# Optimization experiments

Hardware: AMD Instinct MI355X
Metric: run time of the kernel (lower is better)

The kernel has to match this reference:

```python
import jax, jax.numpy as jnp
import numpy as np

N_ACC = 100000   # accounts
N_TX = 300000    # transactions
E = 600000       # edges per edge type
H = 256          # hidden_dim
TX_IN = 32
ACC_IN = 16
L = 2            # conv_layers
M = 300000       # edges to classify
BN_EPS = 1e-5


def setup_inputs() -> dict:
    key = jax.random.key(0)
    ks = jax.random.split(key, 24)
    def nrm(k, shape, scale=1.0):
        return jax.random.normal(k, shape, jnp.float32) * scale
    inp = {}
    inp["x_acc"] = nrm(ks[0], (N_ACC, ACC_IN))
    inp["x_tx"] = nrm(ks[1], (N_TX, TX_IN))
    inp["tx_raw"] = nrm(ks[2], (M, TX_IN))
    # edge type account -> transaction (row0: src account, row1: dst transaction)
    inp["ei_sends"] = jnp.stack([jax.random.randint(ks[3], (E,), 0, N_ACC),
                                 jax.random.randint(ks[4], (E,), 0, N_TX)])
    # edge type transaction -> account
    inp["ei_recv"] = jnp.stack([jax.random.randint(ks[5], (E,), 0, N_TX),
                                jax.random.randint(ks[6], (E,), 0, N_ACC)])
    inp["sender_idx"] = jax.random.randint(ks[7], (M,), 0, N_ACC)
    inp["receiver_idx"] = jax.random.randint(ks[8], (M,), 0, N_ACC)
    # input projections (torch Linear: y = x @ W.T + b)
    inp["W_acc"] = nrm(ks[9], (H, ACC_IN), ACC_IN ** -0.5)
    inp["b_acc"] = jnp.zeros((H,), jnp.float32)
    inp["W_tx"] = nrm(ks[10], (H, TX_IN), TX_IN ** -0.5)
    inp["b_tx"] = jnp.zeros((H,), jnp.float32)
    s = H ** -0.5
    # SAGEConv params per layer: _at = acc->tx edge type, _ta = tx->acc edge type
    # Wl: applied to mean-aggregated neighbor messages (has bias), Wr: root/self weight (no bias)
    inp["Wl_at"] = nrm(ks[11], (L, H, H), s); inp["bl_at"] = jnp.zeros((L, H), jnp.float32)
    inp["Wr_at"] = nrm(ks[12], (L, H, H), s)
    inp["Wl_ta"] = nrm(ks[13], (L, H, H), s); inp["bl_ta"] = jnp.zeros((L, H), jnp.float32)
    inp["Wr_ta"] = nrm(ks[14], (L, H, H), s)
    # shared BatchNorm1d per layer (inference mode: running stats)
    inp["bn_gamma"] = jnp.ones((L, H), jnp.float32)
    inp["bn_beta"] = jnp.zeros((L, H), jnp.float32)
    inp["bn_mean"] = nrm(ks[15], (L, H), 0.1)
    inp["bn_var"] = jax.random.uniform(ks[16], (L, H), jnp.float32, 0.5, 1.5)
    # edge MLP: Linear(2H+TX_IN -> H), ReLU, Linear(H -> 1)
    inp["W1"] = nrm(ks[17], (H, 2 * H + TX_IN), (2 * H + TX_IN) ** -0.5)
    inp["b1"] = jnp.zeros((H,), jnp.float32)
    inp["W2"] = nrm(ks[18], (1, H), s)
    inp["b2"] = jnp.zeros((1,), jnp.float32)
    return inp


def _sage(x_src, x_dst, ei, Wl, bl, Wr):
    # PyG SAGEConv: lin_l(mean_{j in N(i)} x_src[j]) + lin_r(x_dst[i])
    src, dst = ei[0], ei[1]
    n_dst = x_dst.shape[0]
    msg = x_src[src]                                                   # [E, H] gather
    agg = jax.ops.segment_sum(msg, dst, num_segments=n_dst)           # [N_dst, H] scatter-add
    cnt = jax.ops.segment_sum(jnp.ones((ei.shape[1],), x_src.dtype), dst, num_segments=n_dst)
    mean = agg / jnp.maximum(cnt, 1.0)[:, None]
    return mean @ Wl.T + bl + x_dst @ Wr.T


def _bn(v, g, b, m, var):
    return (v - m) * (g * jax.lax.rsqrt(var + BN_EPS)) + b


def reference(x_acc, x_tx, tx_raw, ei_sends, ei_recv, sender_idx, receiver_idx,
              W_acc, b_acc, W_tx, b_tx,
              Wl_at, bl_at, Wr_at, Wl_ta, bl_ta, Wr_ta,
              bn_gamma, bn_beta, bn_mean, bn_var,
              W1, b1, W2, b2):
    acc = jax.nn.relu(x_acc @ W_acc.T + b_acc)
    tx = jax.nn.relu(x_tx @ W_tx.T + b_tx)
    for l in range(L):
        # HeteroConv(aggr='sum'): each node type receives from exactly one edge type here
        tx_new = _sage(acc, tx, ei_sends, Wl_at[l], bl_at[l], Wr_at[l])
        acc_new = _sage(tx, acc, ei_recv, Wl_ta[l], bl_ta[l], Wr_ta[l])
        acc = jax.nn.relu(_bn(acc_new, bn_gamma[l], bn_beta[l], bn_mean[l], bn_var[l]))
        tx = jax.nn.relu(_bn(tx_new, bn_gamma[l], bn_beta[l], bn_mean[l], bn_var[l]))
    h_sender = acc[sender_idx]      # [M, H]
    h_receiver = acc[receiver_idx]  # [M, H]
    edge_repr = jnp.concatenate([h_sender, h_receiver, tx_raw], axis=1)  # [M, 2H+TX_IN]
    h = jax.nn.relu(edge_repr @ W1.T + b1)
    return (h @ W2.T + b2)[:, 0]    # [M]
```

## Files before the change

kernel.cpp:

```cpp
#include <hip/hip_runtime.h>
#include <hip/hip_bf16.h>

#define H 256
#define NACC 100000
#define NTX  300000
#define NE   600000
#define NM   300000

typedef unsigned short u16;
typedef unsigned int u32;
typedef __bf16 bf16x8 __attribute__((ext_vector_type(8)));
typedef float f32x4 __attribute__((ext_vector_type(4)));

__device__ __forceinline__ float bf2f(u32 u) {
    union { u32 i; float f; } v; v.i = u << 16; return v.f;
}
__device__ __forceinline__ u16 f2bf(float f) {
    union { float f; u32 i; } v; v.f = f;
    u32 r = v.i + 0x7FFFu + ((v.i >> 16) & 1u);
    return (u16)(r >> 16);
}
__device__ __forceinline__ u32 pk2(float a, float b) {
    return (u32)f2bf(a) | ((u32)f2bf(b) << 16);
}

__global__ void fillz_kernel(u32* __restrict__ p, long long n) {
    long long i = (long long)blockIdx.x * blockDim.x + threadIdx.x;
    long long st = (long long)gridDim.x * blockDim.x;
    for (; i < n; i += st) p[i] = 0u;
}

__global__ void wcat_kernel(const float* __restrict__ Wl, const float* __restrict__ Wr,
                            u16* __restrict__ dst) {
    int c = blockIdx.x, t = threadIdx.x;
    dst[(size_t)c * 512 + t]       = f2bf(Wl[(size_t)c * 256 + t]);
    dst[(size_t)c * 512 + 256 + t] = f2bf(Wr[(size_t)c * 256 + t]);
}
__global__ void w1cvt_kernel(const float* __restrict__ W1, u16* __restrict__ dst) {
    int c = blockIdx.x, t = threadIdx.x;
    for (int k = t; k < 544; k += 256)
        dst[(size_t)c * 544 + k] = f2bf(W1[(size_t)c * 544 + k]);
}
__global__ void wproj_kernel(const float* __restrict__ W, u16* __restrict__ dst, int K) {
    int c = blockIdx.x, t = threadIdx.x;
    dst[(size_t)c * 32 + t] = (t < K) ? f2bf(W[(size_t)c * K + t]) : (u16)0;
}
__global__ void bnprep_kernel(const float* __restrict__ bl, const float* __restrict__ g,
                              const float* __restrict__ be, const float* __restrict__ m,
                              const float* __restrict__ v,
                              float* __restrict__ S, float* __restrict__ B) {
    int c = threadIdx.x;
    float s = g[c] * rsqrtf(v[c] + 1e-5f);
    S[c] = s;
    B[c] = (bl[c] - m[c]) * s + be[c];
}

template <int KK>
__launch_bounds__(256)
__global__ void proj_mfma(const float* __restrict__ x, const u16* __restrict__ Wb,
                          const float* __restrict__ b, u16* __restrict__ out, int N) {
    __shared__ __align__(16) u16 Af[8][64][8];
    __shared__ __align__(16) u16 Bf[16][64][8];
    int tid = threadIdx.x;
    int w = tid >> 6, lane = tid & 63;
    int row0 = blockIdx.x * 128;
    {
        int r = tid >> 1, h = tid & 1;
        int gr = row0 + r;
        int rt = r >> 4, rr = r & 15;
        uint4 p0 = make_uint4(0, 0, 0, 0), p1 = p0;
        if (gr < N && (KK == 32 || h == 0)) {
            const float* xp = x + (size_t)gr * KK + h * 16;
            float4 f0 = *(const float4*)(xp);
            float4 f1 = *(const float4*)(xp + 4);
            float4 f2 = *(const float4*)(xp + 8);
            float4 f3 = *(const float4*)(xp + 12);
            p0 = make_uint4(pk2(f0.x, f0.y), pk2(f0.z, f0.w), pk2(f1.x, f1.y), pk2(f1.z, f1.w));
            p1 = make_uint4(pk2(f2.x, f2.y), pk2(f2.z, f2.w), pk2(f3.x, f3.y), pk2(f3.z, f3.w));
        }
        int kg0 = 2 * h;
        *(uint4*)(&Af[rt][(kg0 * 16 + rr) ^ (kg0 << 2)][0]) = p0;
        *(uint4*)(&Af[rt][((kg0 + 1) * 16 + rr) ^ ((kg0 + 1) << 2)][0]) = p1;
    }
    {
        const u16* wp = Wb + (size_t)tid * 32;
#pragma unroll
        for (int q = 0; q < 4; ++q) {
            uint4 wv = *(const uint4*)(wp + q * 8);
            *(uint4*)(&Bf[tid >> 4][q * 16 + (tid & 15)][0]) = wv;
        }
    }
    __syncthreads();
    int arslot = lane ^ ((lane >> 4) << 2);
    f32x4 acc[8][4];
#pragma unroll
    for (int rt = 0; rt < 8; ++rt) {
        bf16x8 afr = *(const bf16x8*)(&Af[rt][arslot][0]);
#pragma unroll
        for (int ct = 0; ct < 4; ++ct) {
            bf16x8 bfr = *(const bf16x8*)(&Bf[w * 4 + ct][lane][0]);
            acc[rt][ct] = __builtin_amdgcn_mfma_f32_16x16x32_bf16(
                afr, bfr, (f32x4){0.f, 0.f, 0.f, 0.f}, 0, 0, 0);
        }
    }
    int rb = (lane >> 4) * 4, cc = lane & 15;
#pragma unroll
    for (int ct = 0; ct < 4; ++ct) {
        int cg = (w * 4 + ct) * 16 + cc;
        float bv = b[cg];
#pragma unroll
        for (int rt = 0; rt < 8; ++rt)
#pragma unroll
            for (int q = 0; q < 4; ++q) {
                int r = row0 + rt * 16 + rb + q;
                if (r < N)
                    out[(size_t)r * H + cg] = f2bf(fmaxf(acc[rt][ct][q] + bv, 0.0f));
            }
    }
}

__global__ void count_kernel(const int* __restrict__ dst, int E, int* __restrict__ cnt) {
    int e = blockIdx.x * blockDim.x + threadIdx.x;
    if (e < E) atomicAdd(&cnt[dst[e]], 1);
}
__global__ void scan1_kernel(const int* __restrict__ cnt, int N,
                             int* __restrict__ loc, int* __restrict__ bsum) {
    __shared__ int sh[256];
    int b = blockIdx.x, t = threadIdx.x;
    int base = b * 1024 + t * 4;
    int v0 = (base + 0 < N) ? cnt[base + 0] : 0;
    int v1 = (base + 1 < N) ? cnt[base + 1] : 0;
    int v2 = (base + 2 < N) ? cnt[base + 2] : 0;
    int v3 = (base + 3 < N) ? cnt[base + 3] : 0;
    int s = v0 + v1 + v2 + v3;
    sh[t] = s;
    __syncthreads();
    for (int o = 1; o < 256; o <<= 1) {
        int y = (t >= o) ? sh[t - o] : 0;
        __syncthreads();
        sh[t] += y;
        __syncthreads();
    }
    int run = sh[t] - s;
    if (base + 0 < N) loc[base + 0] = run; run += v0;
    if (base + 1 < N) loc[base + 1] = run; run += v1;
    if (base + 2 < N) loc[base + 2] = run; run += v2;
    if (base + 3 < N) loc[base + 3] = run;
    if (t == 0) bsum[b] = sh[255];
}
__global__ void scan2_kernel(int* __restrict__ bsum, int nb) {
    __shared__ int sh[1024];
    int t = threadIdx.x;
    int v = (t < nb) ? bsum[t] : 0;
    sh[t] = v;
    __syncthreads();
    for (int o = 1; o < 1024; o <<= 1) {
        int y = (t >= o) ? sh[t - o] : 0;
        __syncthreads();
        sh[t] += y;
        __syncthreads();
    }
    if (t < nb) bsum[t] = sh[t] - v;
}
__global__ void scan3_kernel(int* __restrict__ ptr, const int* __restrict__ bsum,
                             int N, int total) {
    int i = blockIdx.x * blockDim.x + threadIdx.x;
    if (i < N) ptr[i] += bsum[i >> 10];
    else if (i == N) ptr[N] = total;
}
__global__ void fillcsr_kernel(const int* __restrict__ src, const int* __restrict__ dst, int E,
                               const int* __restrict__ ptr, int* __restrict__ cur,
                               int* __restrict__ perm) {
    int e = blockIdx.x * blockDim.x + threadIdx.x;
    if (e < E) {
        int d = dst[e];
        int pos = ptr[d] + atomicAdd(&cur[d], 1);
        perm[pos] = src[e];
    }
}

template <int WS>
__launch_bounds__(256)
__global__ void gmean_kernel(const u16* __restrict__ feat, int fstride,
                             const int* __restrict__ ptr, const int* __restrict__ perm,
                             u16* __restrict__ out, int ostride, int c0,
                             int rows, int lo) {
    constexpr int LPD = WS / 4;
    constexpr int DPB = 256 / LPD;
    int g = threadIdx.x / LPD;
    int ln = threadIdx.x % LPD;
    int w = blockIdx.x * DPB + g;
    if (w >= rows) return;
    int d = lo + w;
    int e0 = ptr[d], e1 = ptr[d + 1];
    float a0 = 0.f, a1 = 0.f, a2 = 0.f, a3 = 0.f;
    for (int e = e0; e < e1; ++e) {
        int s = perm[e];
        uint2 v = *(const uint2*)(feat + (size_t)s * fstride + (ln << 2));
        a0 += bf2f(v.x & 0xffff); a1 += bf2f(v.x >> 16);
        a2 += bf2f(v.y & 0xffff); a3 += bf2f(v.y >> 16);
    }
    int deg = e1 - e0;
    float sc = (deg > 0) ? (1.0f / (float)deg) : 0.0f;
    uint2 pk;
    pk.x = pk2(a0 * sc, a1 * sc);
    pk.y = pk2(a2 * sc, a3 * sc);
    *(uint2*)(out + (size_t)w * ostride + c0 + (ln << 2)) = pk;
}

template <int K, int NC>
__launch_bounds__(256)
__global__ void proj2_kernel(const float* __restrict__ x, const float* __restrict__ W,
                             const float* __restrict__ b, u16* __restrict__ out,
                             int N, int c0, int ost) {
    __shared__ float xs[128][K + 4];
    constexpr int NG = 512 / NC;
    constexpr int RPT = 128 / NG;
    int tid = threadIdx.x;
    int row0 = blockIdx.x * 128;
    constexpr int NF4 = 128 * K / 4;
    for (int f = tid; f < NF4; f += 256) {
        int r = f / (K / 4), kq = (f % (K / 4)) * 4;
        int gr = row0 + r;
        float4 v = (gr < N) ? *(const float4*)(x + (size_t)gr * K + kq)
                            : make_float4(0.f, 0.f, 0.f, 0.f);
        *(float4*)&xs[r][kq] = v;
    }
    int lt2 = (tid % (NC / 2)) * 2;
    int g = tid / (NC / 2);
    float wa[K], wb[K];
    const float* wpa = W + (size_t)(c0 + lt2) * K;
#pragma unroll
    for (int k = 0; k < K; k += 4) {
        float4 va = *(const float4*)(wpa + k);
        float4 vb = *(const float4*)(wpa + K + k);
        wa[k] = va.x; wa[k + 1] = va.y; wa[k + 2] = va.z; wa[k + 3] = va.w;
        wb[k] = vb.x; wb[k + 1] = vb.y; wb[k + 2] = vb.z; wb[k + 3] = vb.w;
    }
    float b0 = b[c0 + lt2], b1 = b[c0 + lt2 + 1];
    __syncthreads();
#pragma unroll
    for (int rr = 0; rr < RPT; ++rr) {
        int r = g * RPT + rr;
        int gr = row0 + r;
        float a0 = b0, a1 = b1;
#pragma unroll
        for (int k = 0; k < K; k += 4) {
            float4 xv = *(const float4*)&xs[r][k];
            a0 += xv.x * wa[k] + xv.y * wa[k + 1] + xv.z * wa[k + 2] + xv.w * wa[k + 3];
            a1 += xv.x * wb[k] + xv.y * wb[k + 1] + xv.z * wb[k + 2] + xv.w * wb[k + 3];
        }
        if (gr < N) {
            u32 pk = (u32)f2bf(fmaxf(a0, 0.f)) | ((u32)f2bf(fmaxf(a1, 0.f)) << 16);
            *(u32*)(out + (size_t)gr * ost + lt2) = pk;
        }
    }
}

__launch_bounds__(256)
__global__ void combine_gather(const u16* __restrict__ featG, const int* __restrict__ ptr,
                               const int* __restrict__ perm, const u16* __restrict__ xd,
                               const u16* __restrict__ Wcat,
                               const float* __restrict__ bnS, const float* __restrict__ bnB,
                               u16* __restrict__ outF, int rows) {
    __shared__ __align__(16) u16 Am[8][4][64][8];
    __shared__ __align__(16) u16 Af[4][64][8];
    __shared__ __align__(16) u16 Bf[16][64][8];
    int tid = threadIdx.x;
    int w = tid >> 6, lane = tid & 63;
    int row0 = blockIdx.x * 64;

    {
        int r = tid >> 2, g = tid & 3;
        int grow = row0 + r;
        float s[64];
#pragma unroll
        for (int i = 0; i < 64; ++i) s[i] = 0.0f;
        float inv = 0.0f;
        if (grow < rows) {
            int e0 = ptr[grow], e1 = ptr[grow + 1];
            int dg = e1 - e0;
            inv = (dg > 0) ? 1.0f / (float)dg : 0.0f;
            int e = e0;
            for (; e + 1 < e1; e += 2) {
                int n0 = perm[e], n1 = perm[e + 1];
                const u16* p0 = featG + (size_t)n0 * H + g * 64;
                const u16* p1 = featG + (size_t)n1 * H + g * 64;
#pragma unroll
                for (int q = 0; q < 8; ++q) {
                    uint4 v0 = *(const uint4*)(p0 + q * 8);
                    uint4 v1 = *(const uint4*)(p1 + q * 8);
                    s[q * 8 + 0] += bf2f(v0.x & 0xffff) + bf2f(v1.x & 0xffff);
                    s[q * 8 + 1] += bf2f(v0.x >> 16)    + bf2f(v1.x >> 16);
                    s[q * 8 + 2] += bf2f(v0.y & 0xffff) + bf2f(v1.y & 0xffff);
                    s[q * 8 + 3] += bf2f(v0.y >> 16)    + bf2f(v1.y >> 16);
                    s[q * 8 + 4] += bf2f(v0.z & 0xffff) + bf2f(v1.z & 0xffff);
                    s[q * 8 + 5] += bf2f(v0.z >> 16)    + bf2f(v1.z >> 16);
                    s[q * 8 + 6] += bf2f(v0.w & 0xffff) + bf2f(v1.w & 0xffff);
                    s[q * 8 + 7] += bf2f(v0.w >> 16)    + bf2f(v1.w >> 16);
                }
            }
            if (e < e1) {
                int n0 = perm[e];
                const u16* p0 = featG + (size_t)n0 * H + g * 64;
#pragma unroll
                for (int q = 0; q < 8; ++q) {
                    uint4 v0 = *(const uint4*)(p0 + q * 8);
                    s[q * 8 + 0] += bf2f(v0.x & 0xffff);
                    s[q * 8 + 1] += bf2f(v0.x >> 16);
                    s[q * 8 + 2] += bf2f(v0.y & 0xffff);
                    s[q * 8 + 3] += bf2f(v0.y >> 16);
                    s[q * 8 + 4] += bf2f(v0.z & 0xffff);
                    s[q * 8 + 5] += bf2f(v0.z >> 16);
                    s[q * 8 + 6] += bf2f(v0.w & 0xffff);
                    s[q * 8 + 7] += bf2f(v0.w >> 16);
                }
            }
        }
        int rt = r >> 4, rr = r & 15;
#pragma unroll
        for (int q = 0; q < 8; ++q) {
            int kgg = g * 8 + q;
            int kbs = kgg >> 2, akg = kgg & 3;
            uint4 pv;
            pv.x = pk2(s[q * 8 + 0] * inv, s[q * 8 + 1] * inv);
            pv.y = pk2(s[q * 8 + 2] * inv, s[q * 8 + 3] * inv);
            pv.z = pk2(s[q * 8 + 4] * inv, s[q * 8 + 5] * inv);
            pv.w = pk2(s[q * 8 + 6] * inv, s[q * 8 + 7] * inv);
            *(uint4*)(&Am[kbs][rt][(akg * 16 + rr) ^ (akg << 2)][0]) = pv;
        }
    }

    int arow = tid >> 2, akg = tid & 3;
    int grow = row0 + arow;
    bool arok = grow < rows;
    const u16* ax = xd + (size_t)grow * H;
    int awslot = (akg * 16 + (arow & 15)) ^ (akg << 2);
    int arslot = lane ^ ((lane >> 4) << 2);
    const u16* wp0 = Wcat + (size_t)tid * 512;

    f32x4 acc[4][4];
#pragma unroll
    for (int i = 0; i < 4; ++i)
#pragma unroll
        for (int j = 0; j < 4; ++j) acc[i][j] = (f32x4){0.f, 0.f, 0.f, 0.f};

    for (int kb = 0; kb < 512; kb += 32) {
        if (kb >= 256) {
            uint4 av = make_uint4(0, 0, 0, 0);
            if (arok) av = *(const uint4*)(ax + (kb + akg * 8 - 256));
            *(uint4*)(&Af[arow >> 4][awslot][0]) = av;
        }
#pragma unroll
        for (int q = 0; q < 4; ++q) {
            uint4 wv = *(const uint4*)(wp0 + kb + q * 8);
            *(uint4*)(&Bf[tid >> 4][q * 16 + (tid & 15)][0]) = wv;
        }
        __syncthreads();
        bf16x8 afr[4];
        if (kb < 256) {
            int kbs = kb >> 5;
#pragma unroll
            for (int rt = 0; rt < 4; ++rt)
                afr[rt] = *(const bf16x8*)(&Am[kbs][rt][arslot][0]);
        } else {
#pragma unroll
            for (int rt = 0; rt < 4; ++rt)
                afr[rt] = *(const bf16x8*)(&Af[rt][arslot][0]);
        }
#pragma unroll
        for (int ct = 0; ct < 4; ++ct) {
            bf16x8 bfr = *(const bf16x8*)(&Bf[w * 4 + ct][lane][0]);
#pragma unroll
            for (int rt = 0; rt < 4; ++rt)
                acc[rt][ct] = __builtin_amdgcn_mfma_f32_16x16x32_bf16(afr[rt], bfr, acc[rt][ct], 0, 0, 0);
        }
        __syncthreads();
    }
    int rb = (lane >> 4) * 4, cc = lane & 15;
#pragma unroll
    for (int ct = 0; ct < 4; ++ct) {
        int cg = (w * 4 + ct) * 16 + cc;
        float s = bnS[cg], sh = bnB[cg];
#pragma unroll
        for (int rt = 0; rt < 4; ++rt)
#pragma unroll
            for (int q = 0; q < 4; ++q) {
                int r = row0 + rt * 16 + rb + q;
                if (r < rows)
                    outF[(size_t)r * H + cg] = f2bf(fmaxf(acc[rt][ct][q] * s + sh, 0.0f));
            }
    }
}

template <int COLS>
__launch_bounds__(256)
__global__ void combine_mfma(const u16* __restrict__ mean_, const u16* __restrict__ xd,
                             const u16* __restrict__ Wcat,
                             const float* __restrict__ bnS, const float* __restrict__ bnB,
                             u16* __restrict__ outF, int ostride, int out_c0,
                             int rows, int c0) {
    constexpr int NCT = COLS / 16;
    constexpr int CTW = NCT / 4;
    constexpr int PPT = (COLS * 4) / 256;
    __shared__ __align__(16) u16 Af[4][64][8];
    __shared__ __align__(16) u16 Bf[NCT][64][8];
    int tid = threadIdx.x;
    int w = tid >> 6, lane = tid & 63;
    int row0 = blockIdx.x * 64;
    int arow = tid >> 2, akg = tid & 3;
    bool arok = (row0 + arow) < rows;
    const u16* am = mean_ + (size_t)(row0 + arow) * H;
    const u16* ax = xd + (size_t)(row0 + arow) * H;
    int awslot = (akg * 16 + (arow & 15)) ^ (akg << 2);
    int arslot = lane ^ ((lane >> 4) << 2);
    int bc = tid % COLS;
    int bkg0 = (tid / COLS) * PPT;
    const u16* wp0 = Wcat + (size_t)(c0 + bc) * 512 + bkg0 * 8;

    f32x4 acc[4][CTW];
#pragma unroll
    for (int i = 0; i < 4; ++i)
#pragma unroll
        for (int j = 0; j < CTW; ++j) acc[i][j] = (f32x4){0.f, 0.f, 0.f, 0.f};

    for (int kb = 0; kb < 512; kb += 32) {
        uint4 av = make_uint4(0, 0, 0, 0);
        if (arok) {
            int kg = kb + akg * 8;
            av = (kg < 256) ? *(const uint4*)(am + kg) : *(const uint4*)(ax + (kg - 256));
        }
        *(uint4*)(&Af[arow >> 4][awslot][0]) = av;
#pragma unroll
        for (int q = 0; q < PPT; ++q) {
            uint4 wv = *(const uint4*)(wp0 + kb + q * 8);
            *(uint4*)(&Bf[bc >> 4][(bkg0 + q) * 16 + (bc & 15)][0]) = wv;
        }
        __syncthreads();
        bf16x8 afr[4];
#pragma unroll
        for (int rt = 0; rt < 4; ++rt)
            afr[rt] = *(const bf16x8*)(&Af[rt][arslot][0]);
#pragma unroll
        for (int ctl = 0; ctl < CTW; ++ctl) {
            bf16x8 b = *(const bf16x8*)(&Bf[w * CTW + ctl][lane][0]);
#pragma unroll
            for (int rt = 0; rt < 4; ++rt)
                acc[rt][ctl] = __builtin_amdgcn_mfma_f32_16x16x32_bf16(afr[rt], b, acc[rt][ctl], 0, 0, 0);
        }
        __syncthreads();
    }
    int rb = (lane >> 4) * 4;
    int ccol = lane & 15;
#pragma unroll
    for (int ctl = 0; ctl < CTW; ++ctl) {
        int clocal = (w * CTW + ctl) * 16 + ccol;
        int cg = c0 + clocal;
        float s = bnS[cg], sh = bnB[cg];
#pragma unroll
        for (int rt = 0; rt < 4; ++rt) {
#pragma unroll
            for (int q = 0; q < 4; ++q) {
                int r = row0 + rt * 16 + rb + q;
                if (r < rows)
                    outF[(size_t)r * ostride + out_c0 + clocal] = f2bf(fmaxf(acc[rt][ctl][q] * s + sh, 0.0f));
            }
        }
    }
}

__launch_bounds__(256)
__global__ void mlp_mfma(const u16* __restrict__ accF, const int* __restrict__ sidx,
                         const int* __restrict__ ridx, const float* __restrict__ txr,
                         const u16* __restrict__ W1c, const float* __restrict__ b1,
                         const float* __restrict__ W2, const float* __restrict__ b2,
                         float* __restrict__ out, int M) {
    __shared__ __align__(16) u16 Af[4][64][8];
    __shared__ __align__(16) u16 Bf[16][64][8];
    __shared__ float red[4][64];
    int tid = threadIdx.x;
    int w = tid >> 6, lane = tid & 63;
    int row0 = blockIdx.x * 64;
    int arow = tid >> 2, akg = tid & 3;
    int grow = row0 + arow;
    bool arok = grow < M;
    int si = arok ? sidx[grow] : 0;
    int ri = arok ? ridx[grow] : 0;
    int awslot = (akg * 16 + (arow & 15)) ^ (akg << 2);
    int arslot = lane ^ ((lane >> 4) << 2);
    const u16* wp0 = W1c + (size_t)tid * 544;

    f32x4 acc[4][4];
#pragma unroll
    for (int i = 0; i < 4; ++i)
#pragma unroll
        for (int j = 0; j < 4; ++j) acc[i][j] = (f32x4){0.f, 0.f, 0.f, 0.f};

    for (int kb = 0; kb < 544; kb += 32) {
        uint4 av = make_uint4(0, 0, 0, 0);
        if (arok) {
            int kg = kb + akg * 8;
            if (kg < 256) av = *(const uint4*)(accF + (size_t)si * H + kg);
            else if (kg < 512) av = *(const uint4*)(accF + (size_t)ri * H + (kg - 256));
            else {
                float4 f0 = *(const float4*)(txr + (size_t)grow * 32 + (kg - 512));
                float4 f1 = *(const float4*)(txr + (size_t)grow * 32 + (kg - 512) + 4);
                av.x = pk2(f0.x, f0.y); av.y = pk2(f0.z, f0.w);
                av.z = pk2(f1.x, f1.y); av.w = pk2(f1.z, f1.w);
            }
        }
        *(uint4*)(&Af[arow >> 4][awslot][0]) = av;
#pragma unroll
        for (int q = 0; q < 4; ++q) {
            uint4 wv = *(const uint4*)(wp0 + kb + q * 8);
            *(uint4*)(&Bf[tid >> 4][q * 16 + (tid & 15)][0]) = wv;
        }
        __syncthreads();
        bf16x8 afr[4];
#pragma unroll
        for (int rt = 0; rt < 4; ++rt)
            afr[rt] = *(const bf16x8*)(&Af[rt][arslot][0]);
#pragma unroll
        for (int ctl = 0; ctl < 4; ++ctl) {
            bf16x8 b = *(const bf16x8*)(&Bf[w * 4 + ctl][lane][0]);
#pragma unroll
            for (int rt = 0; rt < 4; ++rt)
                acc[rt][ctl] = __builtin_amdgcn_mfma_f32_16x16x32_bf16(afr[rt], b, acc[rt][ctl], 0, 0, 0);
        }
        __syncthreads();
    }
    float part[4][4];
#pragma unroll
    for (int rt = 0; rt < 4; ++rt)
#pragma unroll
        for (int q = 0; q < 4; ++q) part[rt][q] = 0.0f;
#pragma unroll
    for (int ctl = 0; ctl < 4; ++ctl) {
        int cg = (w * 4 + ctl) * 16 + (lane & 15);
        float b1v = b1[cg], w2v = W2[cg];
#pragma unroll
        for (int rt = 0; rt < 4; ++rt)
#pragma unroll
            for (int q = 0; q < 4; ++q)
                part[rt][q] += fmaxf(acc[rt][ctl][q] + b1v, 0.0f) * w2v;
    }
    int rb = (lane >> 4) * 4;
#pragma unroll
    for (int rt = 0; rt < 4; ++rt)
#pragma unroll
        for (int q = 0; q < 4; ++q) {
            float p = part[rt][q];
            p += __shfl_xor(p, 1);
            p += __shfl_xor(p, 2);
            p += __shfl_xor(p, 4);
            p += __shfl_xor(p, 8);
            if ((lane & 15) == 0) red[w][rt * 16 + rb + q] = p;
        }
    __syncthreads();
    if (tid < 64) {
        int r = row0 + tid;
        if (r < M)
            out[r] = red[0][tid] + red[1][tid] + red[2][tid] + red[3][tid] + b2[0];
    }
}

static inline void fz(void* p, size_t bytes, hipStream_t s) {
    long long n = (long long)(bytes >> 2);
    int g = (int)(((n + 255) / 256 < 2048) ? (n + 255) / 256 : 2048);
    fillz_kernel<<<g, 256, 0, s>>>((u32*)p, n);
}
static inline size_t al256(size_t x) { return (x + 255) & ~(size_t)255; }

extern "C" void kernel_launch(void* const* d_in, const int* in_sizes, int n_in,
                              void* d_out, int out_size, void* d_ws, size_t ws_size,
                              hipStream_t stream) {
    const float* x_acc  = (const float*)d_in[0];
    const float* x_tx   = (const float*)d_in[1];
    const float* tx_raw = (const float*)d_in[2];
    const int* ei_sends = (const int*)d_in[3];
    const int* ei_recv  = (const int*)d_in[4];
    const int* sidx     = (const int*)d_in[5];
    const int* ridx     = (const int*)d_in[6];
    const float* W_acc  = (const float*)d_in[7];
    const float* b_acc  = (const float*)d_in[8];
    const float* W_tx   = (const float*)d_in[9];
    const float* b_tx   = (const float*)d_in[10];
    const float* Wl_at  = (const float*)d_in[11];
    const float* bl_at  = (const float*)d_in[12];
    const float* Wr_at  = (const float*)d_in[13];
    const float* Wl_ta  = (const float*)d_in[14];
    const float* bl_ta  = (const float*)d_in[15];
    const float* Wr_ta  = (const float*)d_in[16];
    const float* bng    = (const float*)d_in[17];
    const float* bnb    = (const float*)d_in[18];
    const float* bnm    = (const float*)d_in[19];
    const float* bnv    = (const float*)d_in[20];
    const float* W1     = (const float*)d_in[21];
    const float* b1     = (const float*)d_in[22];
    const float* W2     = (const float*)d_in[23];
    const float* b2     = (const float*)d_in[24];
    float* out = (float*)d_out;

    const size_t szFeatA = (size_t)NACC * H * 2;
    const size_t szFeatT = (size_t)NTX * H * 2;
    const size_t szCSR = al256((NTX + 1) * 4) + al256(4096) + al256((NTX + 1) * 4)
                       + al256((size_t)NE * 4) + al256((NACC + 1) * 4) + al256((size_t)NE * 4);
    const size_t szW = 3 * al256(256 * 512 * 2) + al256(256 * 544 * 2)
                     + 2 * al256(3 * 256 * 4) + 2 * al256(256 * 32 * 2);

    size_t needF = szCSR + szW + 2 * al256(szFeatA) + al256(szFeatT) + 65536;
    auto needS = [&](int S, int CC) {
        return 3 * al256(szFeatA) + szCSR + szW + 2 * al256((size_t)CC * H * 2)
             + al256((size_t)NTX * (H / S) * 2) + 65536;
    };
    int plan, S = 2, CC = 16384;
    if (needF <= ws_size)                { plan = 0; }
    else if (needS(2, 16384) <= ws_size) { plan = 1; S = 2; CC = 16384; }
    else if (needS(4, 16384) <= ws_size) { plan = 1; S = 4; CC = 16384; }
    else                                 { plan = 1; S = 4; CC = 2048; }

    char* wsp = (char*)d_ws;
    size_t off = 0;
    auto alloc = [&](size_t bytes) -> void* {
        void* p = wsp + off;
        off = al256(off + bytes);
        return p;
    };
    int* cnt   = (int*)alloc((NTX + 1) * 4);
    int* bsum  = (int*)alloc(4096);
    int* ptrT  = (int*)alloc((NTX + 1) * 4);
    int* permS = (int*)alloc((size_t)NE * 4);
    int* ptrA  = (int*)alloc((NACC + 1) * 4);
    int* permR = (int*)alloc((size_t)NE * 4);
    u16* Wc[3];
    Wc[0] = (u16*)alloc(256 * 512 * 2);
    Wc[1] = (u16*)alloc(256 * 512 * 2);
    Wc[2] = (u16*)alloc(256 * 512 * 2);
    u16* W1c = (u16*)alloc(256 * 544 * 2);
    float* bnS = (float*)alloc(3 * 256 * 4);
    float* bnB = (float*)alloc(3 * 256 * 4);
    u16* WbA = (u16*)alloc(256 * 32 * 2);
    u16* WbT = (u16*)alloc(256 * 32 * 2);
    u16* A0f = (u16*)alloc(szFeatA);
    u16* A1f = (u16*)alloc(szFeatA);

    wcat_kernel<<<256, 256, 0, stream>>>(Wl_ta, Wr_ta, Wc[0]);
    wcat_kernel<<<256, 256, 0, stream>>>(Wl_at, Wr_at, Wc[1]);
    wcat_kernel<<<256, 256, 0, stream>>>(Wl_ta + H * H, Wr_ta + H * H, Wc[2]);
    w1cvt_kernel<<<256, 256, 0, stream>>>(W1, W1c);
    wproj_kernel<<<256, 32, 0, stream>>>(W_acc, WbA, 16);
    wproj_kernel<<<256, 32, 0, stream>>>(W_tx, WbT, 32);
    bnprep_kernel<<<1, 256, 0, stream>>>(bl_ta, bng, bnb, bnm, bnv, bnS, bnB);
    bnprep_kernel<<<1, 256, 0, stream>>>(bl_at, bng, bnb, bnm, bnv, bnS + 256, bnB + 256);
    bnprep_kernel<<<1, 256, 0, stream>>>(bl_ta + H, bng + H, bnb + H, bnm + H, bnv + H,
                                         bnS + 512, bnB + 512);

    const int EG = (NE + 255) / 256;
    const int nbT = (NTX + 1023) / 1024, nbA = (NACC + 1023) / 1024;
    fz(cnt, (size_t)NTX * 4, stream);
    count_kernel<<<EG, 256, 0, stream>>>(ei_sends + NE, NE, cnt);
    scan1_kernel<<<nbT, 256, 0, stream>>>(cnt, NTX, ptrT, bsum);
    scan2_kernel<<<1, 1024, 0, stream>>>(bsum, nbT);
    scan3_kernel<<<(NTX + 256) / 256 + 1, 256, 0, stream>>>(ptrT, bsum, NTX, NE);
    fz(cnt, (size_t)NTX * 4, stream);
    fillcsr_kernel<<<EG, 256, 0, stream>>>(ei_sends, ei_sends + NE, NE, ptrT, cnt, permS);
    fz(cnt, (size_t)NACC * 4, stream);
    count_kernel<<<EG, 256, 0, stream>>>(ei_recv + NE, NE, cnt);
    scan1_kernel<<<nbA, 256, 0, stream>>>(cnt, NACC, ptrA, bsum);
    scan2_kernel<<<1, 1024, 0, stream>>>(bsum, nbA);
    scan3_kernel<<<(NACC + 256) / 256 + 1, 256, 0, stream>>>(ptrA, bsum, NACC, NE);
    fz(cnt, (size_t)NACC * 4, stream);
    fillcsr_kernel<<<EG, 256, 0, stream>>>(ei_recv, ei_recv + NE, NE, ptrA, cnt, permR);

    proj_mfma<16><<<(NACC + 127) / 128, 256, 0, stream>>>(x_acc, WbA, b_acc, A0f, NACC);

    const int gA = (NACC + 63) / 64, gM = (NM + 63) / 64;

    if (plan == 0) {
        u16* T = (u16*)alloc(szFeatT);
        proj_mfma<32><<<(NTX + 127) / 128, 256, 0, stream>>>(x_tx, WbT, b_tx, T, NTX);
        combine_gather<<<gA, 256, 0, stream>>>(T, ptrA, permR, A0f, Wc[0], bnS, bnB, A1f, NACC);
        combine_gather<<<(NTX + 63) / 64, 256, 0, stream>>>(A0f, ptrT, permS, T, Wc[1],
                                                            bnS + 256, bnB + 256, T, NTX);
        combine_gather<<<gA, 256, 0, stream>>>(T, ptrA, permR, A1f, Wc[2],
                                               bnS + 512, bnB + 512, A0f, NACC);
        mlp_mfma<<<gM, 256, 0, stream>>>(A0f, sidx, ridx, tx_raw, W1c, b1, W2, b2, out, NM);
    } else {
        u16* meanbuf = (u16*)alloc(szFeatA);
        u16* T0c     = (u16*)alloc((size_t)CC * H * 2);
        u16* meanTc  = (u16*)alloc((size_t)CC * H * 2);
        const int WSL = H / S;
        u16* Tslice  = (u16*)alloc((size_t)NTX * WSL * 2);

        for (int s = 0; s < S; ++s) {
            int c0 = s * WSL;
            if (WSL == 128)
                proj2_kernel<32, 128><<<(NTX + 127) / 128, 256, 0, stream>>>(x_tx, W_tx, b_tx, Tslice, NTX, c0, WSL);
            else
                proj2_kernel<32, 64><<<(NTX + 127) / 128, 256, 0, stream>>>(x_tx, W_tx, b_tx, Tslice, NTX, c0, WSL);
            if (WSL == 128)
                gmean_kernel<128><<<(NACC + 7) / 8, 256, 0, stream>>>(Tslice, WSL, ptrA, permR, meanbuf, H, c0, NACC, 0);
            else
                gmean_kernel<64><<<(NACC + 15) / 16, 256, 0, stream>>>(Tslice, WSL, ptrA, permR, meanbuf, H, c0, NACC, 0);
        }
        combine_mfma<256><<<gA, 256, 0, stream>>>(meanbuf, A0f, Wc[0], bnS, bnB, A1f, H, 0, NACC, 0);
        for (int s = 0; s < S; ++s) {
            int c0 = s * WSL;
            for (int lo = 0; lo < NTX; lo += CC) {
                int cur = (NTX - lo < CC) ? (NTX - lo) : CC;
                proj2_kernel<32, 256><<<(cur + 127) / 128, 256, 0, stream>>>(x_tx + (size_t)lo * 32, W_tx, b_tx, T0c, cur, 0, H);
                gmean_kernel<256><<<(cur + 3) / 4, 256, 0, stream>>>(A0f, H, ptrT, permS, meanTc, H, 0, cur, lo);
                if (WSL == 128)
                    combine_mfma<128><<<(cur + 63) / 64, 256, 0, stream>>>(
                        meanTc, T0c, Wc[1], bnS + 256, bnB + 256,
                        Tslice + (size_t)lo * WSL, WSL, 0, cur, c0);
                else
                    combine_mfma<64><<<(cur + 63) / 64, 256, 0, stream>>>(
                        meanTc, T0c, Wc[1], bnS + 256, bnB + 256,
                        Tslice + (size_t)lo * WSL, WSL, 0, cur, c0);
            }
            if (WSL == 128)
                gmean_kernel<128><<<(NACC + 7) / 8, 256, 0, stream>>>(Tslice, WSL, ptrA, permR, meanbuf, H, c0, NACC, 0);
            else
                gmean_kernel<64><<<(NACC + 15) / 16, 256, 0, stream>>>(Tslice, WSL, ptrA, permR, meanbuf, H, c0, NACC, 0);
        }
        combine_mfma<256><<<gA, 256, 0, stream>>>(meanbuf, A1f, Wc[2], bnS + 512, bnB + 512, A0f, H, 0, NACC, 0);
        mlp_mfma<<<gM, 256, 0, stream>>>(A0f, sidx, ridx, tx_raw, W1c, b1, W2, b2, out, NM);
    }
}
```

Measured before the change: 1.147 ms.

## Pre-swizzle weights into MFMA fragment layout and load B operands directly

Adds kernels that convert the concatenated SAGE weights and W1 into a fragment-ordered bf16 layout, so each lane can load its MFMA B fragment straight from global memory. combine_gather drops its LDS staging for the weights and for the root-feature A tiles, along with the per-k-step barriers, and unrolls the k loop. mlp_mfma also reads W1 fragments directly rather than staging them through LDS. The aim is to cut LDS traffic and synchronization, at the cost of more global/L2 weight reads per wave and uncoalesced row reads for the root features.

```diff
diff --git a/kernel.cpp b/kernel.cpp
--- a/kernel.cpp
+++ b/kernel.cpp
@@ -36,10 +36,20 @@
     dst[(size_t)c * 512 + t]       = f2bf(Wl[(size_t)c * 256 + t]);
     dst[(size_t)c * 512 + 256 + t] = f2bf(Wr[(size_t)c * 256 + t]);
 }
-__global__ void w1cvt_kernel(const float* __restrict__ W1, u16* __restrict__ dst) {
-    int c = blockIdx.x, t = threadIdx.x;
-    for (int k = t; k < 544; k += 256)
-        dst[(size_t)c * 544 + k] = f2bf(W1[(size_t)c * 544 + k]);
+__global__ void wcat_frag_kernel(const float* __restrict__ Wl, const float* __restrict__ Wr,
+                                 u16* __restrict__ dst) {
+    int c = blockIdx.x, k = threadIdx.x;
+    float v = (k < 256) ? Wl[(size_t)c * 256 + k] : Wr[(size_t)c * 256 + (k - 256)];
+    int kstep = k >> 5, kg = (k & 31) >> 3, j = k & 7;
+    dst[(size_t)((kstep * 16 + (c >> 4)) * 64 + kg * 16 + (c & 15)) * 8 + j] = f2bf(v);
+}
+__global__ void w1frag_kernel(const float* __restrict__ W1, u16* __restrict__ dst) {
+    int c = blockIdx.x;
+    for (int k = threadIdx.x; k < 544; k += 256) {
+        float v = W1[(size_t)c * 544 + k];
+        int kstep = k >> 5, kg = (k & 31) >> 3, j = k & 7;
+        dst[(size_t)((kstep * 16 + (c >> 4)) * 64 + kg * 16 + (c & 15)) * 8 + j] = f2bf(v);
+    }
 }
 __global__ void wproj_kernel(const float* __restrict__ W, u16* __restrict__ dst, int K) {
     int c = blockIdx.x, t = threadIdx.x;
@@ -260,12 +270,10 @@
 __launch_bounds__(256)
 __global__ void combine_gather(const u16* __restrict__ featG, const int* __restrict__ ptr,
                                const int* __restrict__ perm, const u16* __restrict__ xd,
-                               const u16* __restrict__ Wcat,
+                               const u16* __restrict__ WcF,
                                const float* __restrict__ bnS, const float* __restrict__ bnB,
                                u16* __restrict__ outF, int rows) {
     __shared__ __align__(16) u16 Am[8][4][64][8];
-    __shared__ __align__(16) u16 Af[4][64][8];
-    __shared__ __align__(16) u16 Bf[16][64][8];
     int tid = threadIdx.x;
     int w = tid >> 6, lane = tid & 63;
     int row0 = blockIdx.x * 64;
@@ -330,14 +338,17 @@
             *(uint4*)(&Am[kbs][rt][(akg * 16 + rr) ^ (akg << 2)][0]) = pv;
         }
     }
-
-    int arow = tid >> 2, akg = tid & 3;
-    int grow = row0 + arow;
-    bool arok = grow < rows;
-    const u16* ax = xd + (size_t)grow * H;
-    int awslot = (akg * 16 + (arow & 15)) ^ (akg << 2);
+    __syncthreads();
+
     int arslot = lane ^ ((lane >> 4) << 2);
-    const u16* wp0 = Wcat + (size_t)tid * 512;
+    const u16* xrow[4];
+#pragma unroll
+    for (int rt = 0; rt < 4; ++rt) {
+        int r = row0 + rt * 16 + (lane & 15);
+        if (r > rows - 1) r = rows - 1;
+        xrow[rt] = xd + (size_t)r * H + (lane >> 4) * 8;
+    }
+    const u16* wbase = WcF + (size_t)(w * 4) * 512 + (size_t)lane * 8;
 
     f32x4 acc[4][4];
 #pragma unroll
@@ -345,38 +356,28 @@
 #pragma unroll
         for (int j = 0; j < 4; ++j) acc[i][j] = (f32x4){0.f, 0.f, 0.f, 0.f};
 
+#pragma unroll 4
     for (int kb = 0; kb < 512; kb += 32) {
-        if (kb >= 256) {
-            uint4 av = make_uint4(0, 0, 0, 0);
-            if (arok) av = *(const uint4*)(ax + (kb + akg * 8 - 256));
-            *(uint4*)(&Af[arow >> 4][awslot][0]) = av;
-        }
-#pragma unroll
-        for (int q = 0; q < 4; ++q) {
-            uint4 wv = *(const uint4*)(wp0 + kb + q * 8);
-            *(uint4*)(&Bf[tid >> 4][q * 16 + (tid & 15)][0]) = wv;
-        }
-        __syncthreads();
+        int kstep = kb >> 5;
         bf16x8 afr[4];
         if (kb < 256) {
-            int kbs = kb >> 5;
 #pragma unroll
             for (int rt = 0; rt < 4; ++rt)
-                afr[rt] = *(const bf16x8*)(&Am[kbs][rt][arslot][0]);
+                afr[rt] = *(const bf16x8*)(&Am[kstep][rt][arslot][0]);
         } else {
 #pragma unroll
             for (int rt = 0; rt < 4; ++rt)
-                afr[rt] = *(const bf16x8*)(&Af[rt][arslot][0]);
+                afr[rt] = *(const bf16x8*)(xrow[rt] + (kb - 256));
         }
 #pragma unroll
         for (int ct = 0; ct < 4; ++ct) {
-            bf16x8 bfr = *(const bf16x8*)(&Bf[w * 4 + ct][lane][0]);
+            bf16x8 bfr = *(const bf16x8*)(wbase + (size_t)(kstep * 16 + ct) * 512);
 #pragma unroll
             for (int rt = 0; rt < 4; ++rt)
                 acc[rt][ct] = __builtin_amdgcn_mfma_f32_16x16x32_bf16(afr[rt], bfr, acc[rt][ct], 0, 0, 0);
         }
-        __syncthreads();
-    }
+    }
+    __syncthreads();
     int rb = (lane >> 4) * 4, cc = lane & 15;
 #pragma unroll
     for (int ct = 0; ct < 4; ++ct) {
@@ -472,11 +473,10 @@
 __launch_bounds__(256)
 __global__ void mlp_mfma(const u16* __restrict__ accF, const int* __restrict__ sidx,
                          const int* __restrict__ ridx, const float* __restrict__ txr,
-                         const u16* __restrict__ W1c, const float* __restrict__ b1,
+                         const u16* __restrict__ W1F, const float* __restrict__ b1,
                          const float* __restrict__ W2, const float* __restrict__ b2,
                          float* __restrict__ out, int M) {
     __shared__ __align__(16) u16 Af[4][64][8];
-    __shared__ __align__(16) u16 Bf[16][64][8];
     __shared__ float red[4][64];
     int tid = threadIdx.x;
     int w = tid >> 6, lane = tid & 63;
@@ -488,7 +488,7 @@
     int ri = arok ? ridx[grow] : 0;
     int awslot = (akg * 16 + (arow & 15)) ^ (akg << 2);
     int arslot = lane ^ ((lane >> 4) << 2);
-    const u16* wp0 = W1c + (size_t)tid * 544;
+    const u16* wbase = W1F + (size_t)(w * 4) * 512 + (size_t)lane * 8;
 
     f32x4 acc[4][4];
 #pragma unroll
@@ -510,22 +510,18 @@
             }
         }
         *(uint4*)(&Af[arow >> 4][awslot][0]) = av;
-#pragma unroll
-        for (int q = 0; q < 4; ++q) {
-            uint4 wv = *(const uint4*)(wp0 + kb + q * 8);
-            *(uint4*)(&Bf[tid >> 4][q * 16 + (tid & 15)][0]) = wv;
-        }
         __syncthreads();
+        int kstep = kb >> 5;
         bf16x8 afr[4];
 #pragma unroll
         for (int rt = 0; rt < 4; ++rt)
             afr[rt] = *(const bf16x8*)(&Af[rt][arslot][0]);
 #pragma unroll
-        for (int ctl = 0; ctl < 4; ++ctl) {
-            bf16x8 b = *(const bf16x8*)(&Bf[w * 4 + ctl][lane][0]);
+        for (int ct = 0; ct < 4; ++ct) {
+            bf16x8 bfr = *(const bf16x8*)(wbase + (size_t)(kstep * 16 + ct) * 512);
 #pragma unroll
             for (int rt = 0; rt < 4; ++rt)
-                acc[rt][ctl] = __builtin_amdgcn_mfma_f32_16x16x32_bf16(afr[rt], b, acc[rt][ctl], 0, 0, 0);
+                acc[rt][ct] = __builtin_amdgcn_mfma_f32_16x16x32_bf16(afr[rt], bfr, acc[rt][ct], 0, 0, 0);
         }
         __syncthreads();
     }
@@ -535,14 +531,14 @@
 #pragma unroll
         for (int q = 0; q < 4; ++q) part[rt][q] = 0.0f;
 #pragma unroll
-    for (int ctl = 0; ctl < 4; ++ctl) {
-        int cg = (w * 4 + ctl) * 16 + (lane & 15);
+    for (int ct = 0; ct < 4; ++ct) {
+        int cg = (w * 4 + ct) * 16 + (lane & 15);
         float b1v = b1[cg], w2v = W2[cg];
 #pragma unroll
         for (int rt = 0; rt < 4; ++rt)
 #pragma unroll
             for (int q = 0; q < 4; ++q)
-                part[rt][q] += fmaxf(acc[rt][ctl][q] + b1v, 0.0f) * w2v;
+                part[rt][q] += fmaxf(acc[rt][ct][q] + b1v, 0.0f) * w2v;
     }
     int rb = (lane >> 4) * 4;
 #pragma unroll
@@ -605,7 +601,8 @@
     const size_t szFeatT = (size_t)NTX * H * 2;
     const size_t szCSR = al256((NTX + 1) * 4) + al256(4096) + al256((NTX + 1) * 4)
                        + al256((size_t)NE * 4) + al256((NACC + 1) * 4) + al256((size_t)NE * 4);
-    const size_t szW = 3 * al256(256 * 512 * 2) + al256(256 * 544 * 2)
+    const size_t szW = 3 * al256(256 * 512 * 2) + 3 * al256(16 * 16 * 64 * 8 * 2)
+                     + al256(17 * 16 * 64 * 8 * 2)
                      + 2 * al256(3 * 256 * 4) + 2 * al256(256 * 32 * 2);
 
     size_t needF = szCSR + szW + 2 * al256(szFeatA) + al256(szFeatT) + 65536;
@@ -636,7 +633,11 @@
     Wc[0] = (u16*)alloc(256 * 512 * 2);
     Wc[1] = (u16*)alloc(256 * 512 * 2);
     Wc[2] = (u16*)alloc(256 * 512 * 2);
-    u16* W1c = (u16*)alloc(256 * 544 * 2);
+    u16* WcF[3];
+    WcF[0] = (u16*)alloc(16 * 16 * 64 * 8 * 2);
+    WcF[1] = (u16*)alloc(16 * 16 * 64 * 8 * 2);
+    WcF[2] = (u16*)alloc(16 * 16 * 64 * 8 * 2);
+    u16* W1F = (u16*)alloc(17 * 16 * 64 * 8 * 2);
     float* bnS = (float*)alloc(3 * 256 * 4);
     float* bnB = (float*)alloc(3 * 256 * 4);
     u16* WbA = (u16*)alloc(256 * 32 * 2);
@@ -647,7 +648,10 @@
     wcat_kernel<<<256, 256, 0, stream>>>(Wl_ta, Wr_ta, Wc[0]);
     wcat_kernel<<<256, 256, 0, stream>>>(Wl_at, Wr_at, Wc[1]);
     wcat_kernel<<<256, 256, 0, stream>>>(Wl_ta + H * H, Wr_ta + H * H, Wc[2]);
-    w1cvt_kernel<<<256, 256, 0, stream>>>(W1, W1c);
+    wcat_frag_kernel<<<256, 512, 0, stream>>>(Wl_ta, Wr_ta, WcF[0]);
+    wcat_frag_kernel<<<256, 512, 0, stream>>>(Wl_at, Wr_at, WcF[1]);
+    wcat_frag_kernel<<<256, 512, 0, stream>>>(Wl_ta + H * H, Wr_ta + H * H, WcF[2]);
+    w1frag_kernel<<<256, 256, 0, stream>>>(W1, W1F);
     wproj_kernel<<<256, 32, 0, stream>>>(W_acc, WbA, 16);
     wproj_kernel<<<256, 32, 0, stream>>>(W_tx, WbT, 32);
     bnprep_kernel<<<1, 256, 0, stream>>>(bl_ta, bng, bnb, bnm, bnv, bnS, bnB);
@@ -679,12 +683,12 @@
     if (plan == 0) {
         u16* T = (u16*)alloc(szFeatT);
         proj_mfma<32><<<(NTX + 127) / 128, 256, 0, stream>>>(x_tx, WbT, b_tx, T, NTX);
-        combine_gather<<<gA, 256, 0, stream>>>(T, ptrA, permR, A0f, Wc[0], bnS, bnB, A1f, NACC);
-        combine_gather<<<(NTX + 63) / 64, 256, 0, stream>>>(A0f, ptrT, permS, T, Wc[1],
+        combine_gather<<<gA, 256, 0, stream>>>(T, ptrA, permR, A0f, WcF[0], bnS, bnB, A1f, NACC);
+        combine_gather<<<(NTX + 63) / 64, 256, 0, stream>>>(A0f, ptrT, permS, T, WcF[1],
                                                             bnS + 256, bnB + 256, T, NTX);
-        combine_gather<<<gA, 256, 0, stream>>>(T, ptrA, permR, A1f, Wc[2],
+        combine_gather<<<gA, 256, 0, stream>>>(T, ptrA, permR, A1f, WcF[2],
                                                bnS + 512, bnB + 512, A0f, NACC);
-        mlp_mfma<<<gM, 256, 0, stream>>>(A0f, sidx, ridx, tx_raw, W1c, b1, W2, b2, out, NM);
+        mlp_mfma<<<gM, 256, 0, stream>>>(A0f, sidx, ridx, tx_raw, W1F, b1, W2, b2, out, NM);
     } else {
         u16* meanbuf = (u16*)alloc(szFeatA);
         u16* T0c     = (u16*)alloc((size_t)CC * H * 2);
@@ -725,6 +729,6 @@
                 gmean_kernel<64><<<(NACC + 15) / 16, 256, 0, stream>>>(Tslice, WSL, ptrA, permR, meanbuf, H, c0, NACC, 0);
         }
         combine_mfma<256><<<gA, 256, 0, stream>>>(meanbuf, A1f, Wc[2], bnS + 512, bnB + 512, A0f, H, 0, NACC, 0);
-        mlp_mfma<<<gM, 256, 0, stream>>>(A0f, sidx, ridx, tx_raw, W1c, b1, W2, b2, out, NM);
-    }
-}
+        mlp_mfma<<<gM, 256, 0, stream>>>(A0f, sidx, ridx, tx_raw, W1F, b1, W2, b2, out, NM);
+    }
+}
```

New measurement: 1.088 ms. -5.1%, faster.
